# Kernel optimization log

Hardware: AMD Instinct MI355X
Metric: run time of the kernel (lower is better)

## Reference

```python
import jax, jax.numpy as jnp
import numpy as np

B, S, D, H = 4, 2048, 1024, 16
DK = D // H


def setup_inputs() -> dict:
    key = jax.random.key(0)
    ks = jax.random.split(key, 12)
    s = 1.0 / np.sqrt(D)
    inp = {
        "q": jax.random.normal(ks[0], (B, S, D), jnp.float32),
        "k": jax.random.normal(ks[1], (B, S, D), jnp.float32),
        "v": jax.random.normal(ks[2], (B, S, D), jnp.float32),
        # causal mask, broadcastable over batch and heads
        "mask": jnp.tril(jnp.ones((S, S), jnp.int32))[None, None, :, :],
        "Wq": jax.random.uniform(ks[3], (D, D), jnp.float32, -s, s),
        "bq": jax.random.uniform(ks[4], (D,), jnp.float32, -s, s),
        "Wk": jax.random.uniform(ks[5], (D, D), jnp.float32, -s, s),
        "bk": jax.random.uniform(ks[6], (D,), jnp.float32, -s, s),
        "Wv": jax.random.uniform(ks[7], (D, D), jnp.float32, -s, s),
        "bv": jax.random.uniform(ks[8], (D,), jnp.float32, -s, s),
        "Wo": jax.random.uniform(ks[9], (D, D), jnp.float32, -s, s),
        "bo": jax.random.uniform(ks[10], (D,), jnp.float32, -s, s),
    }
    return inp


def reference(q, k, v, mask, Wq, bq, Wk, bk, Wv, bv, Wo, bo):
    def split_heads(x):  # [B,S,D] -> [B,H,S,DK]
        return x.reshape(B, S, H, DK).transpose(0, 2, 1, 3)

    qh = split_heads(q @ Wq.T + bq)
    kh = split_heads(k @ Wk.T + bk)
    vh = split_heads(v @ Wv.T + bv)

    scores = jnp.einsum("bhqd,bhkd->bhqk", qh, kh) / jnp.sqrt(jnp.float32(DK))
    scores = jnp.where(mask == 0, jnp.float32(-1e9), scores)
    attn = jax.nn.softmax(scores, axis=-1)
    out = jnp.einsum("bhqk,bhkd->bhqd", attn, vh)
    out = out.transpose(0, 2, 1, 3).reshape(B, S, D)
    return out @ Wo.T + bo
```

## Files before the change

### kernel.cpp

```cpp
#include <hip/hip_runtime.h>
#include <cstdint>

#define Bb 4
#define Ss 2048
#define Dd 1024
#define Hh 16

typedef unsigned short u16;
typedef unsigned int u32;
typedef __attribute__((ext_vector_type(8))) short short8;
typedef __attribute__((ext_vector_type(8))) _Float16 half8;
typedef __attribute__((ext_vector_type(2))) __fp16 fp16x2;
typedef __attribute__((ext_vector_type(4))) float floatx4;
typedef __attribute__((ext_vector_type(16))) float floatx16;
typedef __attribute__((address_space(3))) u32 lds_u32;
typedef const __attribute__((address_space(1))) u32 glob_u32;

__device__ __forceinline__ u16 f2bf(float x) {
  union { float f; u32 u; } v; v.f = x;
  u32 r = v.u + 0x7fffu + ((v.u >> 16) & 1u);
  return (u16)(r >> 16);
}

__device__ __forceinline__ u32 pkbf(float a, float b) {
  u32 r;
  asm("v_cvt_pk_bf16_f32 %0, %1, %2" : "=v"(r) : "v"(a), "v"(b));
  return r;
}

__device__ __forceinline__ u32 pk2(float a, float b) {
  union { fp16x2 h; u32 u; } cv;
  cv.h = __builtin_amdgcn_cvt_pkrtz(a, b);
  return cv.u;
}

__device__ __forceinline__ fp16x2 asH2(u32 x) {
  union { u32 u; fp16x2 h; } c; c.u = x; return c.h;
}

__device__ __forceinline__ half8 h8_from(u32 a, u32 b, u32 c, u32 d) {
  union { u32 u[4]; half8 h; } t;
  t.u[0] = a; t.u[1] = b; t.u[2] = c; t.u[3] = d;
  return t.h;
}

__global__ __launch_bounds__(256) void cvt_many(
    const float* __restrict__ s0, const float* __restrict__ s1,
    const float* __restrict__ s2, const float* __restrict__ s3,
    const float* __restrict__ s4, const float* __restrict__ s5,
    const float* __restrict__ s6, u16* __restrict__ d0, u16* __restrict__ d1,
    u16* __restrict__ d2, u16* __restrict__ d3, u16* __restrict__ d4,
    u16* __restrict__ d5, u16* __restrict__ d6, int nAB, int nWB) {
  int bid = blockIdx.x;
  int z, i0;
  if (bid < 3 * nAB) {
    z = bid / nAB;
    i0 = bid % nAB;
  } else {
    int r = bid - 3 * nAB;
    z = 3 + r / nWB;
    i0 = r % nWB;
  }
  const float* s = z == 0 ? s0 : z == 1 ? s1 : z == 2 ? s2
                   : z == 3 ? s3 : z == 4 ? s4 : z == 5 ? s5 : s6;
  u16* d = z == 0 ? d0 : z == 1 ? d1 : z == 2 ? d2
           : z == 3 ? d3 : z == 4 ? d4 : z == 5 ? d5 : d6;
  int i = i0 * 256 + threadIdx.x;
  const float4* sp = (const float4*)s;
  float4 a = sp[2 * i], b = sp[2 * i + 1];
  u32 w0 = (u32)f2bf(a.x) | ((u32)f2bf(a.y) << 16);
  u32 w1 = (u32)f2bf(a.z) | ((u32)f2bf(a.w) << 16);
  u32 w2 = (u32)f2bf(b.x) | ((u32)f2bf(b.y) << 16);
  u32 w3 = (u32)f2bf(b.z) | ((u32)f2bf(b.w) << 16);
  ((uint4*)d)[i] = make_uint4(w0, w1, w2, w3);
}

__global__ __launch_bounds__(256) void gemm_qkv(const u16* qb, const u16* kb, const u16* vb,
                                                const u16* Wq, const u16* Wk, const u16* Wv,
                                                const float* bq, const float* bk, const float* bv,
                                                u16* qo, u16* ko, _Float16* vT) {
  __shared__ u16 As[128 * 64];
  __shared__ u16 Bs[128 * 64];
  const float K1 = 0.18033688f;
  int z = blockIdx.z;
  const u16* A = z == 0 ? qb : z == 1 ? kb : vb;
  const u16* W = z == 0 ? Wq : z == 1 ? Wk : Wv;
  const float* bias = z == 0 ? bq : z == 1 ? bk : bv;
  float scale = z == 0 ? K1 : 1.0f;

  int tid = threadIdx.x;
  int wave = tid >> 6, lane = tid & 63;
  int quad = lane >> 4, l16 = lane & 15;
  int m0 = blockIdx.x * 128, n0 = blockIdx.y * 128;
  int wr = (wave >> 1) * 64, wc = (wave & 1) * 64;
  int s7 = l16 & 7;
  int srow = wave * 8 + (lane >> 3);
  int gcol = (((lane & 7) ^ (lane >> 3)) << 3);

  floatx4 vzero = {0.f, 0.f, 0.f, 0.f};
  floatx4 acc[4][4];
#pragma unroll
  for (int i = 0; i < 4; ++i)
#pragma unroll
    for (int j = 0; j < 4; ++j) acc[i][j] = vzero;

  for (int kt = 0; kt < Dd; kt += 64) {
    __syncthreads();
#pragma unroll
    for (int c = 0; c < 4; ++c) {
      int r = c * 32 + srow;
      __builtin_amdgcn_global_load_lds(
          (glob_u32*)&A[(size_t)(m0 + r) * Dd + kt + gcol],
          (lds_u32*)&As[(c * 32 + wave * 8) * 64], 16, 0, 0);
      __builtin_amdgcn_global_load_lds(
          (glob_u32*)&W[(size_t)(n0 + r) * Dd + kt + gcol],
          (lds_u32*)&Bs[(c * 32 + wave * 8) * 64], 16, 0, 0);
    }
    __syncthreads();
#pragma unroll
    for (int kk = 0; kk < 2; ++kk) {
      short8 af[4], bf[4];
#pragma unroll
      for (int i = 0; i < 4; ++i)
        af[i] = *(const short8*)&As[(wr + i * 16 + l16) * 64 + (((quad + 4 * kk) ^ s7) << 3)];
#pragma unroll
      for (int j = 0; j < 4; ++j)
        bf[j] = *(const short8*)&Bs[(wc + j * 16 + l16) * 64 + (((quad + 4 * kk) ^ s7) << 3)];
      if (z == 2) {
#pragma unroll
        for (int i = 0; i < 4; ++i)
#pragma unroll
          for (int j = 0; j < 4; ++j)
            acc[i][j] = __builtin_amdgcn_mfma_f32_16x16x32_bf16(af[i], bf[j], acc[i][j], 0, 0, 0);
      } else {
#pragma unroll
        for (int i = 0; i < 4; ++i)
#pragma unroll
          for (int j = 0; j < 4; ++j)
            acc[i][j] = __builtin_amdgcn_mfma_f32_16x16x32_bf16(bf[j], af[i], acc[i][j], 0, 0, 0);
      }
    }
  }

  if (z == 2) {
#pragma unroll
    for (int i = 0; i < 4; ++i) {
#pragma unroll
      for (int j = 0; j < 4; ++j) {
        int n = n0 + wc + j * 16 + l16;
        int h = n >> 6, dk = n & 63;
        int b = m0 >> 11;
        int sb = (m0 + wr + i * 16 + quad * 4) & (Ss - 1);
        union { _Float16 h4[4]; uint2 u2; } pv;
#pragma unroll
        for (int r = 0; r < 4; ++r)
          pv.h4[r] = (_Float16)(acc[i][j][r] + bias[n]);
        *(uint2*)&vT[((size_t)(b * Hh + h) * 64 + dk) * Ss + sb] = pv.u2;
      }
    }
  } else {
    u16* out = z == 0 ? qo : ko;
    int m = m0 + wr + l16;
    int b = m >> 11;
#pragma unroll
    for (int i = 0; i < 4; ++i) {
      int s = (m + i * 16) & (Ss - 1);
#pragma unroll
      for (int j = 0; j < 4; ++j) {
        int nb = n0 + wc + j * 16 + quad * 4;
        float4 bi4 = *(const float4*)&bias[nb];
        int h = nb >> 6, dk = nb & 63;
        u32 lo = pkbf((acc[i][j][0] + bi4.x) * scale, (acc[i][j][1] + bi4.y) * scale);
        u32 hi = pkbf((acc[i][j][2] + bi4.z) * scale, (acc[i][j][3] + bi4.w) * scale);
        *(uint2*)&out[((((size_t)b * Hh + h) * Ss + s) << 6) + dk] = make_uint2(lo, hi);
      }
    }
  }
}

__global__ __launch_bounds__(256) void gemm_out(const u16* __restrict__ A,
                                                const u16* __restrict__ Bw,
                                                const float* __restrict__ bias,
                                                float* __restrict__ o) {
  __shared__ u16 As[128 * 64];
  __shared__ u16 Bs[128 * 64];
  int tid = threadIdx.x;
  int wave = tid >> 6, lane = tid & 63;
  int quad = lane >> 4, l16 = lane & 15;
  int m0 = blockIdx.x * 128, n0 = blockIdx.y * 128;
  int wr = (wave >> 1) * 64, wc = (wave & 1) * 64;
  int s7 = l16 & 7;
  int srow = wave * 8 + (lane >> 3);
  int gcol = (((lane & 7) ^ (lane >> 3)) << 3);

  floatx4 vzero = {0.f, 0.f, 0.f, 0.f};
  floatx4 acc[4][4];
#pragma unroll
  for (int i = 0; i < 4; ++i)
#pragma unroll
    for (int j = 0; j < 4; ++j) acc[i][j] = vzero;

  for (int kt = 0; kt < Dd; kt += 64) {
    __syncthreads();
#pragma unroll
    for (int c = 0; c < 4; ++c) {
      int r = c * 32 + srow;
      __builtin_amdgcn_global_load_lds(
          (glob_u32*)&A[(size_t)(m0 + r) * Dd + kt + gcol],
          (lds_u32*)&As[(c * 32 + wave * 8) * 64], 16, 0, 0);
      __builtin_amdgcn_global_load_lds(
          (glob_u32*)&Bw[(size_t)(n0 + r) * Dd + kt + gcol],
          (lds_u32*)&Bs[(c * 32 + wave * 8) * 64], 16, 0, 0);
    }
    __syncthreads();
#pragma unroll
    for (int kk = 0; kk < 2; ++kk) {
      short8 af[4], bf[4];
#pragma unroll
      for (int i = 0; i < 4; ++i)
        af[i] = *(const short8*)&As[(wr + i * 16 + l16) * 64 + (((quad + 4 * kk) ^ s7) << 3)];
#pragma unroll
      for (int j = 0; j < 4; ++j)
        bf[j] = *(const short8*)&Bs[(wc + j * 16 + l16) * 64 + (((quad + 4 * kk) ^ s7) << 3)];
#pragma unroll
      for (int i = 0; i < 4; ++i)
#pragma unroll
        for (int j = 0; j < 4; ++j)
          acc[i][j] = __builtin_amdgcn_mfma_f32_16x16x32_bf16(bf[j], af[i], acc[i][j], 0, 0, 0);
    }
  }

#pragma unroll
  for (int i = 0; i < 4; ++i) {
    int m = m0 + wr + i * 16 + l16;
#pragma unroll
    for (int j = 0; j < 4; ++j) {
      int nb = n0 + wc + j * 16 + quad * 4;
      float4 bi4 = *(const float4*)&bias[nb];
      float4 val = make_float4(acc[i][j][0] + bi4.x, acc[i][j][1] + bi4.y,
                               acc[i][j][2] + bi4.z, acc[i][j][3] + bi4.w);
      *(float4*)&o[(size_t)m * Dd + nb] = val;
    }
  }
}

#define MFIX 4.0f
#define SW(a, b) asm("v_permlane32_swap_b32 %0, %1" : "+v"(a), "+v"(b))
#define VRD(CH, NT) \
  (*(const half8*)&Vt[p][((NT) * 32 + l31) * 64 + ((((CH) + hi) ^ s7b) << 3)])

#define TILE_BODY(NST, MASKED)                                                \
  do {                                                                        \
    short8 kf0[4], kf1[4];                                                    \
    _Pragma("unroll") for (int m = 0; m < 4; ++m) {                           \
      kf0[m] = *(const short8*)&Kt[p][l31 * 64 + (((2 * m + hi) ^ s7b) << 3)];\
      if (NST == 2)                                                           \
        kf1[m] = *(const short8*)&Kt[p][(32 + l31) * 64 +                     \
                                        (((2 * m + hi) ^ s7b) << 3)];         \
    }                                                                         \
    floatx16 sc0, sc1;                                                        \
    __builtin_amdgcn_s_setprio(1);                                            \
    sc0 = __builtin_amdgcn_mfma_f32_32x32x16_bf16(kf0[0], qf[0], minit, 0, 0, 0); \
    if (NST == 2)                                                             \
      sc1 = __builtin_amdgcn_mfma_f32_32x32x16_bf16(kf1[0], qf[0], minit, 0, 0, 0); \
    _Pragma("unroll") for (int m = 1; m < 4; ++m) {                           \
      sc0 = __builtin_amdgcn_mfma_f32_32x32x16_bf16(kf0[m], qf[m], sc0, 0, 0, 0); \
      if (NST == 2)                                                           \
        sc1 = __builtin_amdgcn_mfma_f32_32x32x16_bf16(kf1[m], qf[m], sc1, 0, 0, 0); \
    }                                                                         \
    __builtin_amdgcn_s_setprio(0);                                            \
    if (MASKED) {                                                             \
      int qrow = Rq + l31;                                                    \
      _Pragma("unroll") for (int r = 0; r < 16; ++r) {                        \
        int key = k0 + 4 * hi + (r & 3) + 8 * (r >> 2);                       \
        if (key > qrow) sc0[r] = -3e38f;                                      \
        if (NST == 2 && key + 32 > qrow) sc1[r] = -3e38f;                     \
      }                                                                       \
    }                                                                         \
    u32 c0[8], c1[8];                                                         \
    _Pragma("unroll") for (int j = 0; j < 8; ++j) {                           \
      c0[j] = pk2(__builtin_amdgcn_exp2f(sc0[2 * j]),                         \
                  __builtin_amdgcn_exp2f(sc0[2 * j + 1]));                    \
      if (NST == 2)                                                           \
        c1[j] = pk2(__builtin_amdgcn_exp2f(sc1[2 * j]),                       \
                    __builtin_amdgcn_exp2f(sc1[2 * j + 1]));                  \
    }                                                                         \
    {                                                                         \
      fp16x2 t0 = asH2(c0[0]) + asH2(c0[1]);                                  \
      fp16x2 t1 = asH2(c0[2]) + asH2(c0[3]);                                  \
      fp16x2 t2 = asH2(c0[4]) + asH2(c0[5]);                                  \
      fp16x2 t3 = asH2(c0[6]) + asH2(c0[7]);                                  \
      fp16x2 ts = (t0 + t1) + (t2 + t3);                                      \
      if (NST == 2) {                                                         \
        fp16x2 u0 = asH2(c1[0]) + asH2(c1[1]);                                \
        fp16x2 u1 = asH2(c1[2]) + asH2(c1[3]);                                \
        fp16x2 u2 = asH2(c1[4]) + asH2(c1[5]);                                \
        fp16x2 u3 = asH2(c1[6]) + asH2(c1[7]);                                \
        ts = ts + ((u0 + u1) + (u2 + u3));                                    \
      }                                                                       \
      l_part += (float)ts[0] + (float)ts[1];                                  \
    }                                                                         \
    SW(c0[0], c0[2]); SW(c0[1], c0[3]); SW(c0[4], c0[6]); SW(c0[5], c0[7]);   \
    if (NST == 2) {                                                           \
      SW(c1[0], c1[2]); SW(c1[1], c1[3]); SW(c1[4], c1[6]); SW(c1[5], c1[7]); \
    }                                                                         \
    __builtin_amdgcn_s_setprio(1);                                            \
    {                                                                         \
      half8 pa = h8_from(c0[0], c0[1], c0[2], c0[3]);                         \
      o0 = __builtin_amdgcn_mfma_f32_32x32x16_f16(pa, VRD(0, 0), o0, 0, 0, 0);\
      o1 = __builtin_amdgcn_mfma_f32_32x32x16_f16(pa, VRD(0, 1), o1, 0, 0, 0);\
      half8 pb = h8_from(c0[4], c0[5], c0[6], c0[7]);                         \
      o0 = __builtin_amdgcn_mfma_f32_32x32x16_f16(pb, VRD(2, 0), o0, 0, 0, 0);\
      o1 = __builtin_amdgcn_mfma_f32_32x32x16_f16(pb, VRD(2, 1), o1, 0, 0, 0);\
      if (NST == 2) {                                                         \
        half8 pc = h8_from(c1[0], c1[1], c1[2], c1[3]);                       \
        o0 = __builtin_amdgcn_mfma_f32_32x32x16_f16(pc, VRD(4, 0), o0, 0, 0, 0); \
        o1 = __builtin_amdgcn_mfma_f32_32x32x16_f16(pc, VRD(4, 1), o1, 0, 0, 0); \
        half8 pd = h8_from(c1[4], c1[5], c1[6], c1[7]);                       \
        o0 = __builtin_amdgcn_mfma_f32_32x32x16_f16(pd, VRD(6, 0), o0, 0, 0, 0); \
        o1 = __builtin_amdgcn_mfma_f32_32x32x16_f16(pd, VRD(6, 1), o1, 0, 0, 0); \
      }                                                                       \
    }                                                                         \
    __builtin_amdgcn_s_setprio(0);                                            \
  } while (0)

__global__ __launch_bounds__(256) void attn_kernel(const u16* __restrict__ qh,
                                                   const u16* __restrict__ kh,
                                                   const _Float16* __restrict__ vT,
                                                   u16* __restrict__ ctx) {
  __shared__ u16 Kt[2][64 * 64];
  __shared__ _Float16 Vt[2][64 * 64];

  int tid = threadIdx.x, w = tid >> 6, lane = tid & 63;
  int hi = lane >> 5, l31 = lane & 31, s7b = lane & 7;
  int bh = blockIdx.x;
  int s = 15 - blockIdx.y;
  const u16* Q = qh + (size_t)bh * Ss * 64;
  const u16* K = kh + (size_t)bh * Ss * 64;
  const _Float16* V = vT + (size_t)bh * 64 * Ss;

  int Rq = 128 * s + 32 * w;

  short8 qf[4];
#pragma unroll
  for (int m = 0; m < 4; ++m)
    qf[m] = *(const short8*)&Q[(size_t)(Rq + l31) * 64 + m * 16 + hi * 8];

  floatx16 minit;
#pragma unroll
  for (int r = 0; r < 16; ++r) minit[r] = -MFIX;
  floatx16 o0, o1;
#pragma unroll
  for (int r = 0; r < 16; ++r) { o0[r] = 0.f; o1[r] = 0.f; }
  float l_part = 0.f;

  int srow = tid >> 3;
  int g8 = ((tid & 7) ^ ((tid >> 3) & 7)) << 3;

#define STAGE(P, KT)                                                          \
  do {                                                                        \
    int _k0 = (KT) * 64;                                                      \
    _Pragma("unroll") for (int c = 0; c < 2; ++c) {                           \
      int r_ = c * 32 + srow;                                                 \
      __builtin_amdgcn_global_load_lds(                                       \
          (glob_u32*)&K[(size_t)(_k0 + r_) * 64 + g8],                        \
          (lds_u32*)&Kt[P][(c * 32 + w * 8) * 64], 16, 0, 0);                 \
      __builtin_amdgcn_global_load_lds(                                       \
          (glob_u32*)&V[(size_t)r_ * Ss + _k0 + g8],                          \
          (lds_u32*)&Vt[P][(c * 32 + w * 8) * 64], 16, 0, 0);                 \
    }                                                                         \
  } while (0)

  STAGE(0, 0);

  int p = 0;
  int nt = 2 * s + 2;
  for (int kt = 0; kt < nt; ++kt) {
    int k0 = kt * 64;
    __syncthreads();
    if (kt + 1 < nt) STAGE(p ^ 1, kt + 1);

    if (k0 + 63 <= Rq) {
      TILE_BODY(2, false);
    } else if (k0 <= Rq + 31) {
      if (k0 + 32 <= Rq + 31) TILE_BODY(2, true);
      else TILE_BODY(1, true);
    }
    p ^= 1;
  }
#undef STAGE

  float l2 = l_part + __shfl_xor(l_part, 32, 64);
  float linv = 1.0f / l2;
  int b = bh >> 4, h = bh & 15;
#pragma unroll
  for (int r = 0; r < 16; ++r) {
    int qi = (r & 3) + 8 * (r >> 2) + 4 * hi;
    float li = __shfl(linv, qi, 64);
    size_t base = ((size_t)b * Ss + Rq + qi) * Dd + h * 64 + l31;
    ctx[base] = f2bf(o0[r] * li);
    ctx[base + 32] = f2bf(o1[r] * li);
  }
}

extern "C" void kernel_launch(void* const* d_in, const int* in_sizes, int n_in,
                              void* d_out, int out_size, void* d_ws, size_t ws_size,
                              hipStream_t stream) {
  const float* q = (const float*)d_in[0];
  const float* k = (const float*)d_in[1];
  const float* v = (const float*)d_in[2];
  const float* Wq = (const float*)d_in[4];
  const float* bq = (const float*)d_in[5];
  const float* Wk = (const float*)d_in[6];
  const float* bk = (const float*)d_in[7];
  const float* Wv = (const float*)d_in[8];
  const float* bv = (const float*)d_in[9];
  const float* Wo = (const float*)d_in[10];
  const float* bo = (const float*)d_in[11];

  char* ws = (char*)d_ws;
  const size_t MB = 1024 * 1024;
  u16* qb = (u16*)(ws + 0 * MB);
  u16* kb = (u16*)(ws + 16 * MB);
  u16* vb = (u16*)(ws + 32 * MB);
  u16* Wqb = (u16*)(ws + 48 * MB);
  u16* Wkb = (u16*)(ws + 50 * MB);
  u16* Wvb = (u16*)(ws + 52 * MB);
  u16* Wob = (u16*)(ws + 54 * MB);
  u16* qhp = (u16*)(ws + 56 * MB);
  u16* khp = (u16*)(ws + 72 * MB);
  _Float16* vhT = (_Float16*)(ws + 88 * MB);
  u16* ctx = qb;

  const int nAB = (Bb * Ss * Dd) / 8 / 256;
  const int nWB = (Dd * Dd) / 8 / 256;
  {
    dim3 g(3 * nAB + 4 * nWB);
    cvt_many<<<g, 256, 0, stream>>>(q, k, v, Wq, Wk, Wv, Wo,
                                    qb, kb, vb, Wqb, Wkb, Wvb, Wob, nAB, nWB);
  }
  {
    dim3 g((Bb * Ss) / 128, Dd / 128, 3);
    gemm_qkv<<<g, 256, 0, stream>>>(qb, kb, vb, Wqb, Wkb, Wvb, bq, bk, bv, qhp, khp, vhT);
  }
  {
    dim3 g(Bb * Hh, 16);
    attn_kernel<<<g, 256, 0, stream>>>(qhp, khp, vhT, ctx);
  }
  {
    dim3 g((Bb * Ss) / 128, Dd / 128);
    gemm_out<<<g, 256, 0, stream>>>(ctx, Wob, bo, (float*)d_out);
  }
}
```

Measured before the change: 314.0 us.

## Rewrite QKV projection GEMM as 256x256 tile, 8-wave, double-buffered pipelined kernel

Replaces the 128x128, 4-wave QKV GEMM with a 256x256 tile computed by 8 waves. The K loop is double-buffered in LDS and staged asynchronously with global_load_lds, interleaving loads with MFMA phases under explicit barriers, vmcnt waits and setprio. The goal is to hide global-load latency behind compute and to raise data reuse per tile. In exchange it needs 128KB of LDS and more accumulator registers, and it leaves fewer blocks (384) to cover the GPU.

```diff
diff --git a/kernel.cpp b/kernel.cpp
--- a/kernel.cpp
+++ b/kernel.cpp
@@ -75,99 +75,154 @@
   ((uint4*)d)[i] = make_uint4(w0, w1, w2, w3);
 }
 
-__global__ __launch_bounds__(256) void gemm_qkv(const u16* qb, const u16* kb, const u16* vb,
-                                                const u16* Wq, const u16* Wk, const u16* Wv,
-                                                const float* bq, const float* bk, const float* bv,
-                                                u16* qo, u16* ko, _Float16* vT) {
-  __shared__ u16 As[128 * 64];
-  __shared__ u16 Bs[128 * 64];
-  const float K1 = 0.18033688f;
-  int z = blockIdx.z;
-  const u16* A = z == 0 ? qb : z == 1 ? kb : vb;
-  const u16* W = z == 0 ? Wq : z == 1 ? Wk : Wv;
-  const float* bias = z == 0 ? bq : z == 1 ? bk : bv;
-  float scale = z == 0 ? K1 : 1.0f;
-
+#define MF16 __builtin_amdgcn_mfma_f32_16x16x32_bf16
+#define QBAR asm volatile("s_barrier" ::: "memory")
+
+template <int SWAP>
+__device__ __forceinline__ void qkv_core(const u16* __restrict__ A,
+                                         const u16* __restrict__ W,
+                                         const float* __restrict__ bias,
+                                         void* __restrict__ Cout, float scale,
+                                         u16* __restrict__ Ab,
+                                         u16* __restrict__ Bbs) {
   int tid = threadIdx.x;
-  int wave = tid >> 6, lane = tid & 63;
+  int w = tid >> 6, lane = tid & 63;
+  int wm = w >> 2, wn = w & 3;
   int quad = lane >> 4, l16 = lane & 15;
-  int m0 = blockIdx.x * 128, n0 = blockIdx.y * 128;
-  int wr = (wave >> 1) * 64, wc = (wave & 1) * 64;
   int s7 = l16 & 7;
-  int srow = wave * 8 + (lane >> 3);
-  int gcol = (((lane & 7) ^ (lane >> 3)) << 3);
+  int m0 = blockIdx.x * 256, n0 = blockIdx.y * 256;
+  int r8 = w * 8 + (lane >> 3);
+  int gc8 = ((lane & 7) ^ (r8 & 7)) << 3;
+
+#define AH(BUF, Q, WMH) (Ab + ((((BUF) * 2 + (Q)) * 2 + (WMH)) * 4096))
+#define BHP(BUF, G) (Bbs + (((BUF) * 2 + (G)) * 8192))
+#define STG_A(BUF, Q, KT)                                                    \
+  do {                                                                       \
+    __builtin_amdgcn_global_load_lds(                                        \
+        (glob_u32*)&A[(size_t)(m0 + (Q) * 64 + r8) * Dd + (KT) * 64 + gc8],  \
+        (lds_u32*)(AH(BUF, Q, 0) + (w * 8) * 64), 16, 0, 0);                 \
+    __builtin_amdgcn_global_load_lds(                                        \
+        (glob_u32*)&A[(size_t)(m0 + 128 + (Q) * 64 + r8) * Dd + (KT) * 64 +  \
+                      gc8],                                                  \
+        (lds_u32*)(AH(BUF, Q, 1) + (w * 8) * 64), 16, 0, 0);                 \
+  } while (0)
+#define STG_B(BUF, G, KT)                                                    \
+  do {                                                                       \
+    __builtin_amdgcn_global_load_lds(                                        \
+        (glob_u32*)&W[(size_t)(n0 + (G) * 128 + r8) * Dd + (KT) * 64 + gc8], \
+        (lds_u32*)(BHP(BUF, G) + (w * 8) * 64), 16, 0, 0);                   \
+    __builtin_amdgcn_global_load_lds(                                        \
+        (glob_u32*)&W[(size_t)(n0 + (G) * 128 + 64 + r8) * Dd + (KT) * 64 +  \
+                      gc8],                                                  \
+        (lds_u32*)(BHP(BUF, G) + (64 + w * 8) * 64), 16, 0, 0);              \
+  } while (0)
+#define RDA(BUF, Q, II, KK)                                                  \
+  (*(const short8*)(AH(BUF, Q, wm) + (((II) * 16 + l16) * 64) +              \
+                    ((((KK) * 4 + quad) ^ s7) << 3)))
+#define RDB(BUF, J, KK)                                                      \
+  (*(const short8*)(BHP(BUF, wn >> 1) +                                      \
+                    (((wn & 1) * 64 + (J) * 16 + l16) * 64) +                \
+                    ((((KK) * 4 + quad) ^ s7) << 3)))
+#define PH_MFMA(BUF_IGNORED, BFA, BFB, IO, JO)                               \
+  do {                                                                       \
+    __builtin_amdgcn_s_setprio(1);                                           \
+    _Pragma("unroll") for (int ii = 0; ii < 4; ++ii) {                       \
+      if (SWAP) {                                                            \
+        acc[(IO) + ii][(JO)] = MF16(BFA[0], af[ii][0], acc[(IO) + ii][(JO)], 0, 0, 0); \
+        acc[(IO) + ii][(JO)] = MF16(BFA[1], af[ii][1], acc[(IO) + ii][(JO)], 0, 0, 0); \
+        acc[(IO) + ii][(JO) + 1] = MF16(BFB[0], af[ii][0], acc[(IO) + ii][(JO) + 1], 0, 0, 0); \
+        acc[(IO) + ii][(JO) + 1] = MF16(BFB[1], af[ii][1], acc[(IO) + ii][(JO) + 1], 0, 0, 0); \
+      } else {                                                               \
+        acc[(IO) + ii][(JO)] = MF16(af[ii][0], BFA[0], acc[(IO) + ii][(JO)], 0, 0, 0); \
+        acc[(IO) + ii][(JO)] = MF16(af[ii][1], BFA[1], acc[(IO) + ii][(JO)], 0, 0, 0); \
+        acc[(IO) + ii][(JO) + 1] = MF16(af[ii][0], BFB[0], acc[(IO) + ii][(JO) + 1], 0, 0, 0); \
+        acc[(IO) + ii][(JO) + 1] = MF16(af[ii][1], BFB[1], acc[(IO) + ii][(JO) + 1], 0, 0, 0); \
+      }                                                                      \
+    }                                                                        \
+    __builtin_amdgcn_s_setprio(0);                                           \
+  } while (0)
 
   floatx4 vzero = {0.f, 0.f, 0.f, 0.f};
-  floatx4 acc[4][4];
-#pragma unroll
-  for (int i = 0; i < 4; ++i)
+  floatx4 acc[8][4];
+#pragma unroll
+  for (int i = 0; i < 8; ++i)
 #pragma unroll
     for (int j = 0; j < 4; ++j) acc[i][j] = vzero;
 
-  for (int kt = 0; kt < Dd; kt += 64) {
-    __syncthreads();
-#pragma unroll
-    for (int c = 0; c < 4; ++c) {
-      int r = c * 32 + srow;
-      __builtin_amdgcn_global_load_lds(
-          (glob_u32*)&A[(size_t)(m0 + r) * Dd + kt + gcol],
-          (lds_u32*)&As[(c * 32 + wave * 8) * 64], 16, 0, 0);
-      __builtin_amdgcn_global_load_lds(
-          (glob_u32*)&W[(size_t)(n0 + r) * Dd + kt + gcol],
-          (lds_u32*)&Bs[(c * 32 + wave * 8) * 64], 16, 0, 0);
-    }
-    __syncthreads();
-#pragma unroll
-    for (int kk = 0; kk < 2; ++kk) {
-      short8 af[4], bf[4];
-#pragma unroll
-      for (int i = 0; i < 4; ++i)
-        af[i] = *(const short8*)&As[(wr + i * 16 + l16) * 64 + (((quad + 4 * kk) ^ s7) << 3)];
-#pragma unroll
-      for (int j = 0; j < 4; ++j)
-        bf[j] = *(const short8*)&Bs[(wc + j * 16 + l16) * 64 + (((quad + 4 * kk) ^ s7) << 3)];
-      if (z == 2) {
-#pragma unroll
-        for (int i = 0; i < 4; ++i)
-#pragma unroll
-          for (int j = 0; j < 4; ++j)
-            acc[i][j] = __builtin_amdgcn_mfma_f32_16x16x32_bf16(af[i], bf[j], acc[i][j], 0, 0, 0);
-      } else {
-#pragma unroll
-        for (int i = 0; i < 4; ++i)
-#pragma unroll
-          for (int j = 0; j < 4; ++j)
-            acc[i][j] = __builtin_amdgcn_mfma_f32_16x16x32_bf16(bf[j], af[i], acc[i][j], 0, 0, 0);
-      }
-    }
-  }
-
-  if (z == 2) {
-#pragma unroll
-    for (int i = 0; i < 4; ++i) {
+  STG_A(0, 0, 0); STG_A(0, 1, 0); STG_B(0, 0, 0); STG_B(0, 1, 0);
+  STG_A(1, 0, 1); STG_B(1, 0, 1); STG_B(1, 1, 1);
+  asm volatile("s_waitcnt vmcnt(6)" ::: "memory");
+  QBAR;
+
+  for (int it = 0; it < 8; ++it) {
+    int t1 = 2 * it + 1, t2 = 2 * it + 2, t3 = 2 * it + 3;
+    bool stg = (it < 7);
+    short8 af[4][2], bf0[2], bf1[2], bf2[2], bf3[2];
+
+#pragma unroll
+    for (int ii = 0; ii < 4; ++ii) { af[ii][0] = RDA(0, 0, ii, 0); af[ii][1] = RDA(0, 0, ii, 1); }
+    bf0[0] = RDB(0, 0, 0); bf0[1] = RDB(0, 0, 1);
+    bf1[0] = RDB(0, 1, 0); bf1[1] = RDB(0, 1, 1);
+    STG_A(1, 1, t1);
+    QBAR;
+    PH_MFMA(0, bf0, bf1, 0, 0);
+    QBAR;
+    bf2[0] = RDB(0, 2, 0); bf2[1] = RDB(0, 2, 1);
+    bf3[0] = RDB(0, 3, 0); bf3[1] = RDB(0, 3, 1);
+    if (stg) STG_A(0, 0, t2);
+    QBAR;
+    PH_MFMA(0, bf2, bf3, 0, 2);
+    QBAR;
+#pragma unroll
+    for (int ii = 0; ii < 4; ++ii) { af[ii][0] = RDA(0, 1, ii, 0); af[ii][1] = RDA(0, 1, ii, 1); }
+    if (stg) STG_B(0, 0, t2);
+    QBAR;
+    PH_MFMA(0, bf2, bf3, 4, 2);
+    QBAR;
+    if (stg) STG_B(0, 1, t2);
+    QBAR;
+    PH_MFMA(0, bf0, bf1, 4, 0);
+    if (stg) asm volatile("s_waitcnt vmcnt(6)" ::: "memory");
+    else     asm volatile("s_waitcnt vmcnt(0)" ::: "memory");
+    QBAR;
+
+#pragma unroll
+    for (int ii = 0; ii < 4; ++ii) { af[ii][0] = RDA(1, 0, ii, 0); af[ii][1] = RDA(1, 0, ii, 1); }
+    bf0[0] = RDB(1, 0, 0); bf0[1] = RDB(1, 0, 1);
+    bf1[0] = RDB(1, 1, 0); bf1[1] = RDB(1, 1, 1);
+    if (stg) STG_A(0, 1, t2);
+    QBAR;
+    PH_MFMA(1, bf0, bf1, 0, 0);
+    QBAR;
+    bf2[0] = RDB(1, 2, 0); bf2[1] = RDB(1, 2, 1);
+    bf3[0] = RDB(1, 3, 0); bf3[1] = RDB(1, 3, 1);
+    if (stg) STG_A(1, 0, t3);
+    QBAR;
+    PH_MFMA(1, bf2, bf3, 0, 2);
+    QBAR;
+#pragma unroll
+    for (int ii = 0; ii < 4; ++ii) { af[ii][0] = RDA(1, 1, ii, 0); af[ii][1] = RDA(1, 1, ii, 1); }
+    if (stg) STG_B(1, 0, t3);
+    QBAR;
+    PH_MFMA(1, bf2, bf3, 4, 2);
+    QBAR;
+    if (stg) STG_B(1, 1, t3);
+    QBAR;
+    PH_MFMA(1, bf0, bf1, 4, 0);
+    if (stg) asm volatile("s_waitcnt vmcnt(6)" ::: "memory");
+    QBAR;
+  }
+
+  if (SWAP) {
+    u16* out = (u16*)Cout;
+    int mBase = m0 + wm * 128 + l16;
+    int b = mBase >> 11;
+#pragma unroll
+    for (int i = 0; i < 8; ++i) {
+      int s = (mBase + i * 16) & (Ss - 1);
 #pragma unroll
       for (int j = 0; j < 4; ++j) {
-        int n = n0 + wc + j * 16 + l16;
-        int h = n >> 6, dk = n & 63;
-        int b = m0 >> 11;
-        int sb = (m0 + wr + i * 16 + quad * 4) & (Ss - 1);
-        union { _Float16 h4[4]; uint2 u2; } pv;
-#pragma unroll
-        for (int r = 0; r < 4; ++r)
-          pv.h4[r] = (_Float16)(acc[i][j][r] + bias[n]);
-        *(uint2*)&vT[((size_t)(b * Hh + h) * 64 + dk) * Ss + sb] = pv.u2;
-      }
-    }
-  } else {
-    u16* out = z == 0 ? qo : ko;
-    int m = m0 + wr + l16;
-    int b = m >> 11;
-#pragma unroll
-    for (int i = 0; i < 4; ++i) {
-      int s = (m + i * 16) & (Ss - 1);
-#pragma unroll
-      for (int j = 0; j < 4; ++j) {
-        int nb = n0 + wc + j * 16 + quad * 4;
+        int nb = n0 + wn * 64 + j * 16 + quad * 4;
         float4 bi4 = *(const float4*)&bias[nb];
         int h = nb >> 6, dk = nb & 63;
         u32 lo = pkbf((acc[i][j][0] + bi4.x) * scale, (acc[i][j][1] + bi4.y) * scale);
@@ -175,7 +230,48 @@
         *(uint2*)&out[((((size_t)b * Hh + h) * Ss + s) << 6) + dk] = make_uint2(lo, hi);
       }
     }
-  }
+  } else {
+    _Float16* vT = (_Float16*)Cout;
+    int b = m0 >> 11;
+#pragma unroll
+    for (int i = 0; i < 8; ++i) {
+#pragma unroll
+      for (int j = 0; j < 4; ++j) {
+        int n = n0 + wn * 64 + j * 16 + l16;
+        int h = n >> 6, dk = n & 63;
+        int sb = (m0 + wm * 128 + i * 16 + quad * 4) & (Ss - 1);
+        union { _Float16 h4[4]; uint2 u2; } pv;
+#pragma unroll
+        for (int r = 0; r < 4; ++r)
+          pv.h4[r] = (_Float16)(acc[i][j][r] + bias[n]);
+        *(uint2*)&vT[((size_t)(b * Hh + h) * 64 + dk) * Ss + sb] = pv.u2;
+      }
+    }
+  }
+#undef AH
+#undef BHP
+#undef STG_A
+#undef STG_B
+#undef RDA
+#undef RDB
+#undef PH_MFMA
+}
+
+__global__ __launch_bounds__(512, 2) void gemm_qkv(const u16* qb, const u16* kb, const u16* vb,
+                                                   const u16* Wq, const u16* Wk, const u16* Wv,
+                                                   const float* bq, const float* bk, const float* bv,
+                                                   u16* qo, u16* ko, _Float16* vT) {
+  __shared__ u16 Ab[2 * 2 * 2 * 4096];
+  __shared__ u16 Bbs[2 * 2 * 8192];
+  const float K1 = 0.18033688f;
+  int z = blockIdx.z;
+  const u16* A = z == 0 ? qb : z == 1 ? kb : vb;
+  const u16* W = z == 0 ? Wq : z == 1 ? Wk : Wv;
+  const float* bi = z == 0 ? bq : z == 1 ? bk : bv;
+  if (z == 2)
+    qkv_core<0>(A, W, bi, (void*)vT, 1.0f, Ab, Bbs);
+  else
+    qkv_core<1>(A, W, bi, z == 0 ? (void*)qo : (void*)ko, z == 0 ? K1 : 1.0f, Ab, Bbs);
 }
 
 __global__ __launch_bounds__(256) void gemm_out(const u16* __restrict__ A,
@@ -440,8 +536,8 @@
                                     qb, kb, vb, Wqb, Wkb, Wvb, Wob, nAB, nWB);
   }
   {
-    dim3 g((Bb * Ss) / 128, Dd / 128, 3);
-    gemm_qkv<<<g, 256, 0, stream>>>(qb, kb, vb, Wqb, Wkb, Wvb, bq, bk, bv, qhp, khp, vhT);
+    dim3 g((Bb * Ss) / 256, Dd / 256, 3);
+    gemm_qkv<<<g, 512, 0, stream>>>(qb, kb, vb, Wqb, Wkb, Wvb, bq, bk, bv, qhp, khp, vhT);
   }
   {
     dim3 g(Bb * Hh, 16);
```

Result: no change. 312.7 us (-0.4%).
